# Kernel optimization log

Measured on AMD Instinct MI355X. Metric: run time of the kernel, lower is better.

Reference implementation:

```python
import jax, jax.numpy as jnp
import numpy as np

B, N, C, H = 1, 1024, 384, 12
DK, DV, P, PV = 16, 16, 4, 4  # scalar key/value dims, query/value points
POINT_KEY_DIM = 4

def setup_inputs() -> dict:
    key = jax.random.key(0)
    ks = jax.random.split(key, 12)
    s = 0.02
    x = jax.random.normal(ks[0], (B, N, C), dtype=jnp.float32)
    # random orthonormal frames via QR
    A = jax.random.normal(ks[1], (B, N, 3, 3), dtype=jnp.float32)
    rotations, _ = jnp.linalg.qr(A)
    translations = jax.random.normal(ks[2], (B, N, 3), dtype=jnp.float32) * 10.0
    Wq  = jax.random.normal(ks[3], (C, H * DK), dtype=jnp.float32) * s
    Wk  = jax.random.normal(ks[4], (C, H * DK), dtype=jnp.float32) * s
    Wv  = jax.random.normal(ks[5], (C, H * DV), dtype=jnp.float32) * s
    Wqp = jax.random.normal(ks[6], (C, H * P * 3), dtype=jnp.float32) * s
    Wkp = jax.random.normal(ks[7], (C, H * P * 3), dtype=jnp.float32) * s
    Wvp = jax.random.normal(ks[8], (C, H * PV * 3), dtype=jnp.float32) * s
    Wout = jax.random.normal(ks[9], (H * DV + H * PV, C), dtype=jnp.float32) * s
    bout = jnp.zeros((C,), dtype=jnp.float32)
    return {"x": x, "rotations": rotations, "translations": translations,
            "Wq": Wq, "Wk": Wk, "Wv": Wv, "Wqp": Wqp, "Wkp": Wkp, "Wvp": Wvp,
            "Wout": Wout, "bout": bout}

def reference(x, rotations, translations, Wq, Wk, Wv, Wqp, Wkp, Wvp, Wout, bout):
    b, n, c = x.shape
    h = H
    # scalar q/k/v: (b,n,h,d)
    qs = (x @ Wq).reshape(b, n, h, DK)
    ks_ = (x @ Wk).reshape(b, n, h, DK)
    vs = (x @ Wv).reshape(b, n, h, DV)
    # local points: (b,n,h,p,3)
    qp = (x @ Wqp).reshape(b, n, h, P, 3)
    kp = (x @ Wkp).reshape(b, n, h, P, 3)
    vp = (x @ Wvp).reshape(b, n, h, PV, 3)
    t = translations[:, :, None, None, :]
    # rotate to global frame
    qpg = jnp.einsum('bnij,bnhpj->bnhpi', rotations, qp) + t
    kpg = jnp.einsum('bnij,bnhpj->bnhpi', rotations, kp) + t
    vpg = jnp.einsum('bnij,bnhpj->bnhpi', rotations, vp) + t
    # scalar attention logits (b,h,i,j)
    attn_scalar = jnp.einsum('bihd,bjhd->bhij', qs, ks_)
    # squared distances summed over points and coords, expanded to avoid (n,n,h,p,3) diff tensor
    q2 = (qpg ** 2).sum((-1, -2))          # (b,n,h)
    k2 = (kpg ** 2).sum((-1, -2))          # (b,n,h)
    qk = jnp.einsum('bihpc,bjhpc->bhij', qpg, kpg)
    dist_sq = (q2.transpose(0, 2, 1)[:, :, :, None]
               + k2.transpose(0, 2, 1)[:, :, None, :]
               - 2.0 * qk)                 # (b,h,i,j)
    gamma = np.sqrt(2.0 / (9.0 * POINT_KEY_DIM)).astype(np.float32)
    inv_sqrt_dk = np.float32(1.0 / np.sqrt(DK))
    logits = (attn_scalar - 0.5 * gamma * dist_sq) * inv_sqrt_dk
    w = jax.nn.softmax(logits, axis=-1)    # (b,h,i,j)
    # scalar output: (b,n,h*dv)
    out_scalar = jnp.einsum('bhij,bjhd->bihd', w, vs).reshape(b, n, h * DV)
    # point output in global frame, then back to local frame of residue i
    out_pts_g = jnp.einsum('bhij,bjhpc->bihpc', w, vpg)   # (b,n,h,pv,3)
    centered = out_pts_g - t
    out_pts_local = jnp.einsum('bnji,bnhpj->bnhpi', rotations, centered)
    out_pts_norm = jnp.sqrt((out_pts_local ** 2).sum(-1)).reshape(b, n, h * PV)
    out = jnp.concatenate([out_scalar, out_pts_norm], axis=-1)
    return out @ Wout + bout
```

## Files before the change

### kernel.cpp

```cpp
#include <hip/hip_runtime.h>
#include <math.h>

#define N_TOK 1024
#define C_DIM 384
#define H_NUM 12
#define PCOLS 1024
#define Q0 0
#define K0 192
#define V0 384
#define QP0 576
#define KP0 720
#define VP0 864
#define ATT_W 240
#define COEF 0.11785113019775792f
#define ISD 0.25f
#define CC2 (COEF * ISD)
#define KV_ROWS 60
#define NZ 4

__global__ __launch_bounds__(256) void k_proj(
    const float* __restrict__ x,
    const float* __restrict__ Wq, const float* __restrict__ Wk, const float* __restrict__ Wv,
    const float* __restrict__ Wqp, const float* __restrict__ Wkp, const float* __restrict__ Wvp,
    float* __restrict__ P)
{
    __shared__ float xs[16][68];
    __shared__ float wsh[16][64];
    int tid = threadIdx.x;
    int i0 = blockIdx.x * 64, c0 = blockIdx.y * 64;
    int lr = tid >> 2, lk = (tid & 3) * 4;
    int wr = tid >> 4, wc = (tid & 15) * 4;
    int ty = tid >> 4, tx = tid & 15;

    int col = c0 + wc;
    const float* Wb; int od, cb;
    if (col < 192)       { Wb = Wq;  od = 192; cb = col; }
    else if (col < 384)  { Wb = Wk;  od = 192; cb = col - 192; }
    else if (col < 576)  { Wb = Wv;  od = 192; cb = col - 384; }
    else if (col < 720)  { Wb = Wqp; od = 144; cb = col - 576; }
    else if (col < 864)  { Wb = Wkp; od = 144; cb = col - 720; }
    else if (col < 1008) { Wb = Wvp; od = 144; cb = col - 864; }
    else                 { Wb = nullptr; od = 0; cb = 0; }

    float4 xa = *(const float4*)(x + (i0 + lr) * C_DIM + lk);
    float4 wa = Wb ? *(const float4*)(Wb + wr * od + cb) : make_float4(0.f, 0.f, 0.f, 0.f);
    float acc[4][4] = {};

    for (int it = 0; it < 24; ++it) {
        xs[lk + 0][lr] = xa.x; xs[lk + 1][lr] = xa.y;
        xs[lk + 2][lr] = xa.z; xs[lk + 3][lr] = xa.w;
        *(float4*)&wsh[wr][wc] = wa;
        __syncthreads();
        if (it < 23) {
            xa = *(const float4*)(x + (i0 + lr) * C_DIM + (it + 1) * 16 + lk);
            wa = Wb ? *(const float4*)(Wb + ((it + 1) * 16 + wr) * od + cb)
                    : make_float4(0.f, 0.f, 0.f, 0.f);
        }
#pragma unroll
        for (int kk = 0; kk < 16; ++kk) {
            float4 a = *(float4*)&xs[kk][ty * 4];
            float4 b = *(float4*)&wsh[kk][tx * 4];
            acc[0][0] = fmaf(a.x, b.x, acc[0][0]); acc[0][1] = fmaf(a.x, b.y, acc[0][1]);
            acc[0][2] = fmaf(a.x, b.z, acc[0][2]); acc[0][3] = fmaf(a.x, b.w, acc[0][3]);
            acc[1][0] = fmaf(a.y, b.x, acc[1][0]); acc[1][1] = fmaf(a.y, b.y, acc[1][1]);
            acc[1][2] = fmaf(a.y, b.z, acc[1][2]); acc[1][3] = fmaf(a.y, b.w, acc[1][3]);
            acc[2][0] = fmaf(a.z, b.x, acc[2][0]); acc[2][1] = fmaf(a.z, b.y, acc[2][1]);
            acc[2][2] = fmaf(a.z, b.z, acc[2][2]); acc[2][3] = fmaf(a.z, b.w, acc[2][3]);
            acc[3][0] = fmaf(a.w, b.x, acc[3][0]); acc[3][1] = fmaf(a.w, b.y, acc[3][1]);
            acc[3][2] = fmaf(a.w, b.z, acc[3][2]); acc[3][3] = fmaf(a.w, b.w, acc[3][3]);
        }
        __syncthreads();
    }
#pragma unroll
    for (int r = 0; r < 4; ++r)
        *(float4*)(P + (i0 + ty * 4 + r) * PCOLS + c0 + tx * 4) =
            make_float4(acc[r][0], acc[r][1], acc[r][2], acc[r][3]);
}

__global__ __launch_bounds__(256) void k_prep(
    const float* __restrict__ P, const float* __restrict__ rot, const float* __restrict__ trans,
    float* __restrict__ KVg, float* __restrict__ Qg, float* __restrict__ qcg)
{
    __shared__ float kb[29 * 128];
    __shared__ float qb[29 * 128];
    __shared__ float vb[28 * 128];
    __shared__ float qcb[128];
    int h = blockIdx.y, nb = blockIdx.x;
    int tid = threadIdx.x;
    int nl = tid & 127, role = tid >> 7;
    int n = nb * 128 + nl;
    const float* R = rot + n * 9;
    float R00 = R[0], R01 = R[1], R02 = R[2];
    float R10 = R[3], R11 = R[4], R12 = R[5];
    float R20 = R[6], R21 = R[7], R22 = R[8];
    float t0 = trans[n * 3 + 0], t1 = trans[n * 3 + 1], t2 = trans[n * 3 + 2];

    if (role == 0) {
        const float* kr = P + n * PCOLS + K0 + h * 16;
#pragma unroll
        for (int d = 0; d < 16; ++d) kb[d * 128 + nl] = kr[d];
        const float* kp = P + n * PCOLS + KP0 + h * 12;
        float k2 = 0.f;
#pragma unroll
        for (int pt = 0; pt < 4; ++pt) {
            float p0 = kp[pt * 3 + 0], p1 = kp[pt * 3 + 1], p2 = kp[pt * 3 + 2];
            float g0 = R00 * p0 + R01 * p1 + R02 * p2 + t0;
            float g1 = R10 * p0 + R11 * p1 + R12 * p2 + t1;
            float g2 = R20 * p0 + R21 * p1 + R22 * p2 + t2;
            kb[(16 + pt * 3 + 0) * 128 + nl] = g0;
            kb[(16 + pt * 3 + 1) * 128 + nl] = g1;
            kb[(16 + pt * 3 + 2) * 128 + nl] = g2;
            k2 += g0 * g0 + g1 * g1 + g2 * g2;
        }
        kb[28 * 128 + nl] = -CC2 * k2;
    } else {
        const float* qr = P + n * PCOLS + Q0 + h * 16;
#pragma unroll
        for (int d = 0; d < 16; ++d) qb[d * 128 + nl] = qr[d] * ISD;
        const float* qp = P + n * PCOLS + QP0 + h * 12;
        float q2 = 0.f;
#pragma unroll
        for (int pt = 0; pt < 4; ++pt) {
            float p0 = qp[pt * 3 + 0], p1 = qp[pt * 3 + 1], p2 = qp[pt * 3 + 2];
            float g0 = R00 * p0 + R01 * p1 + R02 * p2 + t0;
            float g1 = R10 * p0 + R11 * p1 + R12 * p2 + t1;
            float g2 = R20 * p0 + R21 * p1 + R22 * p2 + t2;
            qb[(16 + pt * 3 + 0) * 128 + nl] = g0 * (2.f * CC2);
            qb[(16 + pt * 3 + 1) * 128 + nl] = g1 * (2.f * CC2);
            qb[(16 + pt * 3 + 2) * 128 + nl] = g2 * (2.f * CC2);
            q2 += g0 * g0 + g1 * g1 + g2 * g2;
        }
        qb[28 * 128 + nl] = 1.0f;
        qcb[nl] = fmaf(-CC2, q2, -4.0f);
        const float* vr = P + n * PCOLS + V0 + h * 16;
#pragma unroll
        for (int d = 0; d < 16; ++d) vb[d * 128 + nl] = vr[d];
        const float* vp = P + n * PCOLS + VP0 + h * 12;
#pragma unroll
        for (int pt = 0; pt < 4; ++pt) {
            float p0 = vp[pt * 3 + 0], p1 = vp[pt * 3 + 1], p2 = vp[pt * 3 + 2];
            vb[(16 + pt * 3 + 0) * 128 + nl] = R00 * p0 + R01 * p1 + R02 * p2 + t0;
            vb[(16 + pt * 3 + 1) * 128 + nl] = R10 * p0 + R11 * p1 + R12 * p2 + t1;
            vb[(16 + pt * 3 + 2) * 128 + nl] = R20 * p0 + R21 * p1 + R22 * p2 + t2;
        }
    }
    __syncthreads();

    for (int u = tid; u < 57 * 32; u += 256) {
        int d = u >> 5, c4 = u & 31;
        float4 v = (d < 29) ? *(float4*)&kb[d * 128 + c4 * 4]
                            : *(float4*)&vb[(d - 29) * 128 + c4 * 4];
        *(float4*)&KVg[(h * KV_ROWS + d) * 1024 + nb * 128 + c4 * 4] = v;
    }
    for (int u = tid; u < 29 * 32; u += 256) {
        int d = u >> 5, c4 = u & 31;
        *(float4*)&Qg[(h * 29 + d) * 1024 + nb * 128 + c4 * 4] = *(float4*)&qb[d * 128 + c4 * 4];
    }
    if (tid < 32) *(float4*)&qcg[h * 1024 + nb * 128 + tid * 4] = *(float4*)&qcb[tid * 4];
}

__global__ __launch_bounds__(256, 2) void k_attn(
    const float* __restrict__ KVg, const float* __restrict__ Qg,
    const float* __restrict__ qcg, float* __restrict__ part)
{
    __shared__ float KV[2][KV_ROWS * 64];
    __shared__ float red[29 * 64];
    int tid = threadIdx.x;
    int lane = tid & 63, w = tid >> 6;
    int ty = tid >> 3, tx = tid & 7;

    int bid = blockIdx.x;
    int xcd = bid & 7, slot = bid >> 3;
    int pair = xcd * 6 + (slot >> 4);
    int bx = slot & 15;
    int h = pair % H_NUM;
    int z = pair / H_NUM;

    int i0 = bx * 64;
    int jz0 = z * 256;
    const float* KVh = KVg + h * KV_ROWS * 1024;

    float q0[29], q1[29];
#pragma unroll
    for (int d = 0; d < 29; ++d) {
        float2 qv = *(const float2*)&Qg[(h * 29 + d) * 1024 + i0 + ty * 2];
        q0[d] = qv.x; q1[d] = qv.y;
    }
    float qc[2];
    {
        float2 qcv = *(const float2*)&qcg[h * 1024 + i0 + ty * 2];
        qc[0] = qcv.x; qc[1] = qcv.y;
    }

    int nst = (w < 3) ? 4 : 3;
#define STAGE(T) do { float* buf_ = KV[(T) & 1]; int j0_ = jz0 + (T) * 64;        \
        for (int m_ = 0; m_ < nst; ++m_) {                                        \
            int g_ = w * 4 + m_;                                                  \
            const float* src_ = KVh + (g_ * 4 + (lane >> 4)) * 1024 + j0_ + (lane & 15) * 4; \
            float* dst_ = buf_ + g_ * 256;                                        \
            __builtin_amdgcn_global_load_lds(                                     \
                (const __attribute__((address_space(1))) void*)src_,              \
                (__attribute__((address_space(3))) void*)dst_, 16, 0, 0);         \
        } } while (0)

    STAGE(0);
    __syncthreads();

    float out[2][28] = {};
    float denom[2] = {};

    for (int t = 0; t < 4; ++t) {
        if (t < 3) STAGE(t + 1);
        const float* Kb = KV[t & 1];
        const float* Vb = Kb + 29 * 64;

        float s[2][8] = {};
#pragma unroll
        for (int d = 0; d < 29; ++d) {
            float4 k0 = *(const float4*)&Kb[d * 64 + tx * 8];
            float4 k1 = *(const float4*)&Kb[d * 64 + tx * 8 + 4];
            float ka[8] = {k0.x, k0.y, k0.z, k0.w, k1.x, k1.y, k1.z, k1.w};
#pragma unroll
            for (int j = 0; j < 8; ++j) {
                s[0][j] = fmaf(q0[d], ka[j], s[0][j]);
                s[1][j] = fmaf(q1[d], ka[j], s[1][j]);
            }
        }

        float p[2][8];
#pragma unroll
        for (int r = 0; r < 2; ++r) {
#pragma unroll
            for (int j = 0; j < 8; ++j) {
                p[r][j] = __expf(s[r][j] + qc[r]);
                denom[r] += p[r][j];
            }
        }

#pragma unroll
        for (int d = 0; d < 28; ++d) {
            float4 v0 = *(const float4*)&Vb[d * 64 + tx * 8];
            float4 v1 = *(const float4*)&Vb[d * 64 + tx * 8 + 4];
            float va[8] = {v0.x, v0.y, v0.z, v0.w, v1.x, v1.y, v1.z, v1.w};
#pragma unroll
            for (int r = 0; r < 2; ++r) {
                float acc = out[r][d];
#pragma unroll
                for (int j = 0; j < 8; ++j) acc = fmaf(p[r][j], va[j], acc);
                out[r][d] = acc;
            }
        }
        __syncthreads();
    }

#pragma unroll
    for (int m = 1; m <= 4; m <<= 1) {
#pragma unroll
        for (int r = 0; r < 2; ++r) {
#pragma unroll
            for (int d = 0; d < 28; ++d) out[r][d] += __shfl_xor(out[r][d], m, 64);
            denom[r] += __shfl_xor(denom[r], m, 64);
        }
    }
    if (tx == 0) {
#pragma unroll
        for (int r = 0; r < 2; ++r) {
#pragma unroll
            for (int d = 0; d < 28; ++d) red[d * 64 + ty * 2 + r] = out[r][d];
            red[28 * 64 + ty * 2 + r] = denom[r];
        }
    }
    __syncthreads();
    for (int u = tid; u < 29 * 64; u += 256) {
        part[((z * H_NUM + h) * 29 + (u >> 6)) * N_TOK + i0 + (u & 63)] = red[u];
    }
}

__global__ __launch_bounds__(256) void k_comb(
    const float* __restrict__ part, const float* __restrict__ rot,
    const float* __restrict__ trans, float* __restrict__ att)
{
    int t = blockIdx.x * 256 + threadIdx.x;
    int h = t >> 10, i = t & 1023;
    float v[29];
#pragma unroll
    for (int c = 0; c < 29; ++c) {
        float s = 0.f;
#pragma unroll
        for (int z = 0; z < NZ; ++z)
            s += part[((z * H_NUM + h) * 29 + c) * N_TOK + i];
        v[c] = s;
    }
    float inv = 1.f / v[28];
    float* arow = att + i * ATT_W;
#pragma unroll
    for (int d = 0; d < 16; ++d) arow[h * 16 + d] = v[d] * inv;
    float t0 = trans[i * 3 + 0], t1 = trans[i * 3 + 1], t2v = trans[i * 3 + 2];
    const float* R = rot + i * 9;
#pragma unroll
    for (int p = 0; p < 4; ++p) {
        float c0 = v[16 + p * 3 + 0] * inv - t0;
        float c1 = v[16 + p * 3 + 1] * inv - t1;
        float c2 = v[16 + p * 3 + 2] * inv - t2v;
        float l0 = R[0] * c0 + R[3] * c1 + R[6] * c2;
        float l1 = R[1] * c0 + R[4] * c1 + R[7] * c2;
        float l2 = R[2] * c0 + R[5] * c1 + R[8] * c2;
        arow[192 + h * 4 + p] = sqrtf(l0 * l0 + l1 * l1 + l2 * l2);
    }
}

__global__ __launch_bounds__(256) void k_out(
    const float* __restrict__ att, const float* __restrict__ Wout,
    const float* __restrict__ bout, float* __restrict__ out)
{
    __shared__ float xs[64][17];
    __shared__ float wsh[16][64];
    int tid = threadIdx.x;
    int i0 = blockIdx.x * 64, c0 = blockIdx.y * 64;
    int lr = tid >> 2, lk = (tid & 3) * 4;
    int wr = tid >> 4, wc = (tid & 15) * 4;
    int ty = tid >> 4, tx = tid & 15;

    float4 xa = *(const float4*)(att + (i0 + lr) * ATT_W + lk);
    float4 wa = *(const float4*)(Wout + wr * C_DIM + c0 + wc);
    float acc[4][4] = {};

    for (int it = 0; it < 15; ++it) {
        xs[lr][lk + 0] = xa.x; xs[lr][lk + 1] = xa.y;
        xs[lr][lk + 2] = xa.z; xs[lr][lk + 3] = xa.w;
        *(float4*)&wsh[wr][wc] = wa;
        __syncthreads();
        if (it < 14) {
            xa = *(const float4*)(att + (i0 + lr) * ATT_W + (it + 1) * 16 + lk);
            wa = *(const float4*)(Wout + ((it + 1) * 16 + wr) * C_DIM + c0 + wc);
        }
#pragma unroll
        for (int kk = 0; kk < 16; ++kk) {
            float4 b = *(float4*)&wsh[kk][tx * 4];
            float a0 = xs[ty * 4 + 0][kk];
            float a1 = xs[ty * 4 + 1][kk];
            float a2 = xs[ty * 4 + 2][kk];
            float a3 = xs[ty * 4 + 3][kk];
            acc[0][0] = fmaf(a0, b.x, acc[0][0]); acc[0][1] = fmaf(a0, b.y, acc[0][1]);
            acc[0][2] = fmaf(a0, b.z, acc[0][2]); acc[0][3] = fmaf(a0, b.w, acc[0][3]);
            acc[1][0] = fmaf(a1, b.x, acc[1][0]); acc[1][1] = fmaf(a1, b.y, acc[1][1]);
            acc[1][2] = fmaf(a1, b.z, acc[1][2]); acc[1][3] = fmaf(a1, b.w, acc[1][3]);
            acc[2][0] = fmaf(a2, b.x, acc[2][0]); acc[2][1] = fmaf(a2, b.y, acc[2][1]);
            acc[2][2] = fmaf(a2, b.z, acc[2][2]); acc[2][3] = fmaf(a2, b.w, acc[2][3]);
            acc[3][0] = fmaf(a3, b.x, acc[3][0]); acc[3][1] = fmaf(a3, b.y, acc[3][1]);
            acc[3][2] = fmaf(a3, b.z, acc[3][2]); acc[3][3] = fmaf(a3, b.w, acc[3][3]);
        }
        __syncthreads();
    }
    float4 bb = *(const float4*)(bout + c0 + tx * 4);
#pragma unroll
    for (int r = 0; r < 4; ++r) {
        *(float4*)(out + (i0 + ty * 4 + r) * C_DIM + c0 + tx * 4) =
            make_float4(acc[r][0] + bb.x, acc[r][1] + bb.y, acc[r][2] + bb.z, acc[r][3] + bb.w);
    }
}

extern "C" void kernel_launch(void* const* d_in, const int* in_sizes, int n_in,
                              void* d_out, int out_size, void* d_ws, size_t ws_size,
                              hipStream_t stream) {
    const float* x     = (const float*)d_in[0];
    const float* rot   = (const float*)d_in[1];
    const float* trans = (const float*)d_in[2];
    const float* Wq    = (const float*)d_in[3];
    const float* Wk    = (const float*)d_in[4];
    const float* Wv    = (const float*)d_in[5];
    const float* Wqp   = (const float*)d_in[6];
    const float* Wkp   = (const float*)d_in[7];
    const float* Wvp   = (const float*)d_in[8];
    const float* Wout  = (const float*)d_in[9];
    const float* bout  = (const float*)d_in[10];
    float* out = (float*)d_out;

    float* ws  = (float*)d_ws;
    float* P    = ws;
    float* KVg  = P    + N_TOK * PCOLS;
    float* Qg   = KVg  + H_NUM * KV_ROWS * 1024;
    float* qcg  = Qg   + H_NUM * 29 * 1024;
    float* part = qcg  + H_NUM * 1024;
    float* att  = part + NZ * H_NUM * 29 * 1024;

    k_proj<<<dim3(16, 16), 256, 0, stream>>>(x, Wq, Wk, Wv, Wqp, Wkp, Wvp, P);
    k_prep<<<dim3(8, 12), 256, 0, stream>>>(P, rot, trans, KVg, Qg, qcg);
    k_attn<<<768, 256, 0, stream>>>(KVg, Qg, qcg, part);
    k_comb<<<48, 256, 0, stream>>>(part, rot, trans, att);
    k_out<<<dim3(16, 6), 256, 0, stream>>>(att, Wout, bout, out);
}
```

Baseline: 85.61 us.

## Use packed fp16 dot2 for attention logits and scalar value accumulation

Packs Q, K and scalar V into half2 pairs and computes logits and scalar-value sums with v_dot2 (fp16 inputs, fp32 accumulate). The k2 bias is added separately in fp32, and point values stay fp32. The global KV layout becomes per-64-token contiguous tiles so each stage is a single linear copy into LDS. The goal is to halve LDS/global traffic and the FMA count in the attention inner loops. The cost is fp16 rounding of Q/K/V and the softmax weights, which may hurt accuracy.

```diff
diff --git a/kernel.cpp b/kernel.cpp
--- a/kernel.cpp
+++ b/kernel.cpp
@@ -15,8 +15,23 @@
 #define COEF 0.11785113019775792f
 #define ISD 0.25f
 #define CC2 (COEF * ISD)
-#define KV_ROWS 60
 #define NZ 4
+#define OKV_V16 896
+#define OKV_VP 1408
+#define OKV_K2 2176
+#define TILE_U 2240
+#define TILE_PAD 2304
+
+typedef _Float16 f16x2 __attribute__((ext_vector_type(2)));
+typedef __fp16   p16x2 __attribute__((ext_vector_type(2)));
+union U32H2 { unsigned int u; f16x2 f; p16x2 p; };
+__device__ __forceinline__ f16x2 as_h2(unsigned int v) { U32H2 x; x.u = v; return x.f; }
+__device__ __forceinline__ unsigned int pkh(float a, float b) {
+    U32H2 x; x.p = __builtin_amdgcn_cvt_pkrtz(a, b); return x.u;
+}
+__device__ __forceinline__ f16x2 pkf(float a, float b) {
+    U32H2 x; x.p = __builtin_amdgcn_cvt_pkrtz(a, b); return x.f;
+}
 
 __global__ __launch_bounds__(256) void k_proj(
     const float* __restrict__ x,
@@ -79,10 +94,10 @@
 
 __global__ __launch_bounds__(256) void k_prep(
     const float* __restrict__ P, const float* __restrict__ rot, const float* __restrict__ trans,
-    float* __restrict__ KVg, float* __restrict__ Qg, float* __restrict__ qcg)
+    unsigned int* __restrict__ KVT, unsigned int* __restrict__ Qh, float* __restrict__ qcg)
 {
     __shared__ float kb[29 * 128];
-    __shared__ float qb[29 * 128];
+    __shared__ float qb[28 * 128];
     __shared__ float vb[28 * 128];
     __shared__ float qcb[128];
     int h = blockIdx.y, nb = blockIdx.x;
@@ -130,7 +145,6 @@
             qb[(16 + pt * 3 + 2) * 128 + nl] = g2 * (2.f * CC2);
             q2 += g0 * g0 + g1 * g1 + g2 * g2;
         }
-        qb[28 * 128 + nl] = 1.0f;
         qcb[nl] = fmaf(-CC2, q2, -4.0f);
         const float* vr = P + n * PCOLS + V0 + h * 16;
 #pragma unroll
@@ -146,24 +160,41 @@
     }
     __syncthreads();
 
-    for (int u = tid; u < 57 * 32; u += 256) {
-        int d = u >> 5, c4 = u & 31;
-        float4 v = (d < 29) ? *(float4*)&kb[d * 128 + c4 * 4]
-                            : *(float4*)&vb[(d - 29) * 128 + c4 * 4];
-        *(float4*)&KVg[(h * KV_ROWS + d) * 1024 + nb * 128 + c4 * 4] = v;
-    }
-    for (int u = tid; u < 29 * 32; u += 256) {
-        int d = u >> 5, c4 = u & 31;
-        *(float4*)&Qg[(h * 29 + d) * 1024 + nb * 128 + c4 * 4] = *(float4*)&qb[d * 128 + c4 * 4];
+    for (int u = tid; u < 2 * TILE_PAD; u += 256) {
+        int tt = u / TILE_PAD, r = u % TILE_PAD;
+        unsigned int val;
+        if (r < OKV_V16) {
+            int dp = r >> 6, j = r & 63;
+            val = pkh(kb[(2 * dp) * 128 + tt * 64 + j], kb[(2 * dp + 1) * 128 + tt * 64 + j]);
+        } else if (r < OKV_VP) {
+            int idx = r - OKV_V16;
+            int d = idx >> 5, jp = idx & 31;
+            val = pkh(vb[d * 128 + tt * 64 + 2 * jp], vb[d * 128 + tt * 64 + 2 * jp + 1]);
+        } else if (r < OKV_K2) {
+            int idx = r - OKV_VP;
+            int d = idx >> 6, j = idx & 63;
+            val = __float_as_uint(vb[(16 + d) * 128 + tt * 64 + j]);
+        } else if (r < TILE_U) {
+            int j = r - OKV_K2;
+            val = __float_as_uint(kb[28 * 128 + tt * 64 + j]);
+        } else {
+            val = 0u;
+        }
+        KVT[(h * 16 + nb * 2 + tt) * TILE_PAD + r] = val;
+    }
+    for (int u = tid; u < 14 * 128; u += 256) {
+        int dp = u >> 7, n2 = u & 127;
+        Qh[(h * 14 + dp) * 1024 + nb * 128 + n2] =
+            pkh(qb[(2 * dp) * 128 + n2], qb[(2 * dp + 1) * 128 + n2]);
     }
     if (tid < 32) *(float4*)&qcg[h * 1024 + nb * 128 + tid * 4] = *(float4*)&qcb[tid * 4];
 }
 
 __global__ __launch_bounds__(256, 2) void k_attn(
-    const float* __restrict__ KVg, const float* __restrict__ Qg,
+    const unsigned int* __restrict__ KVT, const unsigned int* __restrict__ Qh,
     const float* __restrict__ qcg, float* __restrict__ part)
 {
-    __shared__ float KV[2][KV_ROWS * 64];
+    __shared__ unsigned int KV[2][TILE_PAD];
     __shared__ float red[29 * 64];
     int tid = threadIdx.x;
     int lane = tid & 63, w = tid >> 6;
@@ -177,14 +208,13 @@
     int z = pair / H_NUM;
 
     int i0 = bx * 64;
-    int jz0 = z * 256;
-    const float* KVh = KVg + h * KV_ROWS * 1024;
-
-    float q0[29], q1[29];
-#pragma unroll
-    for (int d = 0; d < 29; ++d) {
-        float2 qv = *(const float2*)&Qg[(h * 29 + d) * 1024 + i0 + ty * 2];
-        q0[d] = qv.x; q1[d] = qv.y;
+    const unsigned int* KVbase = KVT + (h * 16 + z * 4) * TILE_PAD;
+
+    f16x2 q0p[14], q1p[14];
+#pragma unroll
+    for (int dp = 0; dp < 14; ++dp) {
+        q0p[dp] = as_h2(Qh[(h * 14 + dp) * 1024 + i0 + ty * 2 + 0]);
+        q1p[dp] = as_h2(Qh[(h * 14 + dp) * 1024 + i0 + ty * 2 + 1]);
     }
     float qc[2];
     {
@@ -192,15 +222,17 @@
         qc[0] = qcv.x; qc[1] = qcv.y;
     }
 
-    int nst = (w < 3) ? 4 : 3;
-#define STAGE(T) do { float* buf_ = KV[(T) & 1]; int j0_ = jz0 + (T) * 64;        \
-        for (int m_ = 0; m_ < nst; ++m_) {                                        \
-            int g_ = w * 4 + m_;                                                  \
-            const float* src_ = KVh + (g_ * 4 + (lane >> 4)) * 1024 + j0_ + (lane & 15) * 4; \
-            float* dst_ = buf_ + g_ * 256;                                        \
-            __builtin_amdgcn_global_load_lds(                                     \
-                (const __attribute__((address_space(1))) void*)src_,              \
-                (__attribute__((address_space(3))) void*)dst_, 16, 0, 0);         \
+    int nst = (w == 0) ? 3 : 2;
+    int gbase = (w == 0) ? 0 : 1 + w * 2;
+#define STAGE(T) do { unsigned int* buf_ = KV[(T) & 1];                          \
+        const unsigned int* sb_ = KVbase + (T) * TILE_PAD;                       \
+        for (int m_ = 0; m_ < nst; ++m_) {                                       \
+            int g_ = gbase + m_;                                                 \
+            const unsigned int* src_ = sb_ + g_ * 256 + lane * 4;                \
+            unsigned int* dst_ = buf_ + g_ * 256;                                \
+            __builtin_amdgcn_global_load_lds(                                    \
+                (const __attribute__((address_space(1))) void*)src_,             \
+                (__attribute__((address_space(3))) void*)dst_, 16, 0, 0);        \
         } } while (0)
 
     STAGE(0);
@@ -211,43 +243,66 @@
 
     for (int t = 0; t < 4; ++t) {
         if (t < 3) STAGE(t + 1);
-        const float* Kb = KV[t & 1];
-        const float* Vb = Kb + 29 * 64;
+        const unsigned int* Kb = KV[t & 1];
 
         float s[2][8] = {};
 #pragma unroll
-        for (int d = 0; d < 29; ++d) {
-            float4 k0 = *(const float4*)&Kb[d * 64 + tx * 8];
-            float4 k1 = *(const float4*)&Kb[d * 64 + tx * 8 + 4];
-            float ka[8] = {k0.x, k0.y, k0.z, k0.w, k1.x, k1.y, k1.z, k1.w};
+        for (int dp = 0; dp < 14; ++dp) {
+            uint4 a = *(const uint4*)&Kb[dp * 64 + tx * 8];
+            uint4 b = *(const uint4*)&Kb[dp * 64 + tx * 8 + 4];
+            unsigned int ka[8] = {a.x, a.y, a.z, a.w, b.x, b.y, b.z, b.w};
 #pragma unroll
             for (int j = 0; j < 8; ++j) {
-                s[0][j] = fmaf(q0[d], ka[j], s[0][j]);
-                s[1][j] = fmaf(q1[d], ka[j], s[1][j]);
+                s[0][j] = __builtin_amdgcn_fdot2(q0p[dp], as_h2(ka[j]), s[0][j], false);
+                s[1][j] = __builtin_amdgcn_fdot2(q1p[dp], as_h2(ka[j]), s[1][j], false);
             }
         }
+        const float* k2p = (const float*)&Kb[OKV_K2];
+        float4 c0 = *(const float4*)&k2p[tx * 8];
+        float4 c1 = *(const float4*)&k2p[tx * 8 + 4];
+        float k2v[8] = {c0.x, c0.y, c0.z, c0.w, c1.x, c1.y, c1.z, c1.w};
 
         float p[2][8];
 #pragma unroll
         for (int r = 0; r < 2; ++r) {
 #pragma unroll
             for (int j = 0; j < 8; ++j) {
-                p[r][j] = __expf(s[r][j] + qc[r]);
+                p[r][j] = __expf(s[r][j] + k2v[j] + qc[r]);
                 denom[r] += p[r][j];
             }
         }
-
-#pragma unroll
-        for (int d = 0; d < 28; ++d) {
-            float4 v0 = *(const float4*)&Vb[d * 64 + tx * 8];
-            float4 v1 = *(const float4*)&Vb[d * 64 + tx * 8 + 4];
-            float va[8] = {v0.x, v0.y, v0.z, v0.w, v1.x, v1.y, v1.z, v1.w};
+        f16x2 pp[2][4];
+#pragma unroll
+        for (int r = 0; r < 2; ++r)
+#pragma unroll
+            for (int jp = 0; jp < 4; ++jp)
+                pp[r][jp] = pkf(p[r][2 * jp], p[r][2 * jp + 1]);
+
+#pragma unroll
+        for (int d = 0; d < 16; ++d) {
+            uint4 vv = *(const uint4*)&Kb[OKV_V16 + d * 32 + tx * 4];
 #pragma unroll
             for (int r = 0; r < 2; ++r) {
                 float acc = out[r][d];
+                acc = __builtin_amdgcn_fdot2(pp[r][0], as_h2(vv.x), acc, false);
+                acc = __builtin_amdgcn_fdot2(pp[r][1], as_h2(vv.y), acc, false);
+                acc = __builtin_amdgcn_fdot2(pp[r][2], as_h2(vv.z), acc, false);
+                acc = __builtin_amdgcn_fdot2(pp[r][3], as_h2(vv.w), acc, false);
+                out[r][d] = acc;
+            }
+        }
+#pragma unroll
+        for (int d = 0; d < 12; ++d) {
+            const float* vp = (const float*)&Kb[OKV_VP + d * 64];
+            float4 v0 = *(const float4*)&vp[tx * 8];
+            float4 v1 = *(const float4*)&vp[tx * 8 + 4];
+            float va[8] = {v0.x, v0.y, v0.z, v0.w, v1.x, v1.y, v1.z, v1.w};
+#pragma unroll
+            for (int r = 0; r < 2; ++r) {
+                float acc = out[r][16 + d];
 #pragma unroll
                 for (int j = 0; j < 8; ++j) acc = fmaf(p[r][j], va[j], acc);
-                out[r][d] = acc;
+                out[r][16 + d] = acc;
             }
         }
         __syncthreads();
@@ -376,17 +431,17 @@
     const float* bout  = (const float*)d_in[10];
     float* out = (float*)d_out;
 
-    float* ws  = (float*)d_ws;
-    float* P    = ws;
-    float* KVg  = P    + N_TOK * PCOLS;
-    float* Qg   = KVg  + H_NUM * KV_ROWS * 1024;
-    float* qcg  = Qg   + H_NUM * 29 * 1024;
-    float* part = qcg  + H_NUM * 1024;
-    float* att  = part + NZ * H_NUM * 29 * 1024;
+    float* ws = (float*)d_ws;
+    float* P            = ws;
+    unsigned int* KVT   = (unsigned int*)(P + N_TOK * PCOLS);
+    unsigned int* Qh    = KVT + H_NUM * 16 * TILE_PAD;
+    float* qcg          = (float*)(Qh + H_NUM * 14 * 1024);
+    float* part         = qcg + H_NUM * 1024;
+    float* att          = part + NZ * H_NUM * 29 * 1024;
 
     k_proj<<<dim3(16, 16), 256, 0, stream>>>(x, Wq, Wk, Wv, Wqp, Wkp, Wvp, P);
-    k_prep<<<dim3(8, 12), 256, 0, stream>>>(P, rot, trans, KVg, Qg, qcg);
-    k_attn<<<768, 256, 0, stream>>>(KVg, Qg, qcg, part);
+    k_prep<<<dim3(8, 12), 256, 0, stream>>>(P, rot, trans, KVT, Qh, qcg);
+    k_attn<<<768, 256, 0, stream>>>(KVT, Qh, qcg, part);
     k_comb<<<48, 256, 0, stream>>>(part, rot, trans, att);
     k_out<<<dim3(16, 6), 256, 0, stream>>>(att, Wout, bout, out);
 }
```

After: 84.44 us. No clear change (-1.4%).
